# Performance work log

Hardware: AMD Instinct MI355X
Metric: run time of the kernel (lower is better)

Reference implementation:

```python
import jax, jax.numpy as jnp
import numpy as np

D, H, FFN_D, B, LT, LS = 1024, 16, 4096, 4, 1024, 1024
EPS = 1e-5  # torch LayerNorm default
NEG = -10000000000.0


def setup_inputs() -> dict:
    key = jax.random.key(0)
    ks = iter(jax.random.split(key, 64))
    s = 0.02
    n = lambda shape: jax.random.normal(next(ks), shape, jnp.float32) * s
    inp = {
        'enc_output': n((LS, B, D)),
        'embedded': n((LT, B, D)),
        'src_mask': jnp.zeros((LS, B), jnp.bool_),
        'tgt_mask': jnp.zeros((LT, B), jnp.bool_),
    }
    for p in ('mmha', 'ed'):
        for w in ('q', 'k', 'v', 'o'):
            inp[f'{p}_w{w}'] = n((D, D))
            inp[f'{p}_b{w}'] = jnp.zeros((D,), jnp.float32)
    inp['ffn_w1'] = n((FFN_D, D)); inp['ffn_b1'] = jnp.zeros((FFN_D,), jnp.float32)
    inp['ffn_w2'] = n((D, FFN_D)); inp['ffn_b2'] = jnp.zeros((D,), jnp.float32)
    for i in range(3):
        inp[f'ln{i}_g'] = jnp.ones((D,), jnp.float32)
        inp[f'ln{i}_b'] = jnp.zeros((D,), jnp.float32)
    return inp


def _ln(x, g, b):
    m = x.mean(-1, keepdims=True)
    v = ((x - m) ** 2).mean(-1, keepdims=True)
    return (x - m) / jnp.sqrt(v + EPS) * g + b


def _mha(qx, kx, vx, wq, bq, wk, bk, wv, bv, wo, bo, mask):
    # qx: (Lq,B,D); kx,vx: (Lk,B,D); mask broadcastable to (B,H,Lq,Lk), True=masked
    Lq, Bn, Dm = qx.shape
    dk = Dm // H
    proj = lambda x, w, bb: (x @ w.T + bb).reshape(x.shape[0], Bn, H, dk).transpose(1, 2, 0, 3)
    q, k, v = proj(qx, wq, bq), proj(kx, wk, bk), proj(vx, wv, bv)  # (B,H,L,dk)
    scores = jnp.einsum('bhqd,bhkd->bhqk', q, k) / np.float32(np.sqrt(dk))
    scores = jnp.where(mask, NEG, scores)  # masked_fill semantics
    w = jax.nn.softmax(scores, axis=-1)  # dropout is identity in eval
    attn = jnp.einsum('bhqk,bhkd->bhqd', w, v).transpose(2, 0, 1, 3).reshape(Lq, Bn, Dm)
    return attn @ wo.T + bo


def reference(enc_output, embedded, src_mask, tgt_mask,
              mmha_wq, mmha_bq, mmha_wk, mmha_bk, mmha_wv, mmha_bv, mmha_wo, mmha_bo,
              ed_wq, ed_bq, ed_wk, ed_bk, ed_wv, ed_bv, ed_wo, ed_bo,
              ffn_w1, ffn_b1, ffn_w2, ffn_b2,
              ln0_g, ln0_b, ln1_g, ln1_b, ln2_g, ln2_b):
    Lt = embedded.shape[0]
    causal = jnp.triu(jnp.ones((Lt, Lt), jnp.bool_), 1)[None, None]      # (1,1,Lt,Lt)
    tmask = tgt_mask.T[:, None, None, :]                                  # (B,1,1,Lt)
    # Sublayer 0: masked self-attention (computed but UNUSED downstream,
    # faithfully mirroring the original forward which discards self_attn).
    self_attn = embedded + _mha(_ln(embedded, ln0_g, ln0_b), _ln(embedded, ln0_g, ln0_b), _ln(embedded, ln0_g, ln0_b),
                                mmha_wq, mmha_bq, mmha_wk, mmha_bk, mmha_wv, mmha_bv, mmha_wo, mmha_bo,
                                causal | tmask)
    del self_attn
    # Sublayer 1: enc-dec attention; residual input is `embedded` (as in source).
    smask = src_mask.T[:, None, None, :]                                  # (B,1,1,Ls)
    q_in = _ln(embedded, ln1_g, ln1_b)
    enc_dec = embedded + _mha(q_in, enc_output, enc_output,
                              ed_wq, ed_bq, ed_wk, ed_bk, ed_wv, ed_bv, ed_wo, ed_bo,
                              smask)
    # Sublayer 2: FFN
    z = _ln(enc_dec, ln2_g, ln2_b)
    ffn = jnp.maximum(z @ ffn_w1.T + ffn_b1, 0.0) @ ffn_w2.T + ffn_b2
    return enc_dec + ffn
```

## Files before the change

kernel.cpp:

```cpp
#include <hip/hip_runtime.h>
#include <cstdint>
#include <math.h>

constexpr int NH  = 16;
constexpr int DKH = 64;
constexpr int SEQ = 1024;
constexpr int NB  = 4;
constexpr int DM  = 1024;
constexpr int DF  = 4096;

typedef __bf16 bf16;
typedef __bf16 bf16x4 __attribute__((ext_vector_type(4)));
typedef __bf16 bf16x8 __attribute__((ext_vector_type(8)));
typedef float  f32x4  __attribute__((ext_vector_type(4)));

#define MFMA16(a, b, c) __builtin_amdgcn_mfma_f32_16x16x32_bf16((a), (b), (c), 0, 0, 0)

__device__ __forceinline__ void gload_lds16(const void* g, void* l) {
  __builtin_amdgcn_global_load_lds(
      (const __attribute__((address_space(1))) unsigned int*)(uintptr_t)g,
      (__attribute__((address_space(3))) unsigned int*)(uintptr_t)l,
      16, 0, 0);
}

template <int N>
__device__ __forceinline__ void wait_vmcnt() {
  if constexpr (N == 0)      asm volatile("s_waitcnt vmcnt(0)" ::: "memory");
  else if constexpr (N == 3) asm volatile("s_waitcnt vmcnt(3)" ::: "memory");
  else if constexpr (N == 4) asm volatile("s_waitcnt vmcnt(4)" ::: "memory");
  else if constexpr (N == 6) asm volatile("s_waitcnt vmcnt(6)" ::: "memory");
  else                       asm volatile("s_waitcnt vmcnt(8)" ::: "memory");
}

__device__ __forceinline__ int swz32(int row) { return (row >> 1) & 3; }

template <int ROWS>
__device__ __forceinline__ void stage_tile32(const bf16* __restrict__ g, int ldg,
                                             bf16* __restrict__ l, int t) {
  constexpr int ITER = ROWS * 32 / 2048;
#pragma unroll
  for (int i = 0; i < ITER; ++i) {
    const int off = (i * 256 + t) * 8;
    const int row = off >> 5;
    const int cc = (off & 31) >> 3;
    const int sc = cc ^ swz32(row);
    gload_lds16(&g[(size_t)row * ldg + (sc << 3)], &l[off]);
  }
}

__device__ __forceinline__ int rpk(int row, int col) {
  return row * 256 + ((((col >> 3) ^ (row & 7)) << 4)) + ((col & 7) << 1);
}

__global__ __launch_bounds__(256) void prep_kernel(
    const float* __restrict__ wq, const float* __restrict__ wk,
    const float* __restrict__ wv, const float* __restrict__ wo,
    const float* __restrict__ w1, const float* __restrict__ w2,
    const float* __restrict__ enc, const float* __restrict__ emb,
    const float* __restrict__ g1, const float* __restrict__ be1,
    bf16* __restrict__ wqkv_bf, bf16* __restrict__ wo_bf,
    bf16* __restrict__ w1_bf, bf16* __restrict__ w2_bf,
    bf16* __restrict__ enc_bf, bf16* __restrict__ qin_bf) {
  const int bid = blockIdx.x, t = threadIdx.x;
  if (bid < 16384) {
    const float* in;
    bf16* out;
    int idx;
    if (bid < 4096) {
      const int sel = bid >> 10;
      in = sel == 0 ? wq : sel == 1 ? wk : sel == 2 ? wv : wo;
      out = sel == 3 ? wo_bf : wqkv_bf + ((size_t)sel << 20);
      idx = (bid & 1023) * 256 + t;
    } else {
      const int sel = (bid - 4096) >> 12;
      in = sel == 0 ? w1 : sel == 1 ? w2 : enc;
      out = sel == 0 ? w1_bf : sel == 1 ? w2_bf : enc_bf;
      idx = ((bid - 4096) & 4095) * 256 + t;
    }
    const float4 v = ((const float4*)in)[idx];
    bf16x4 ov;
    ov[0] = (bf16)v.x; ov[1] = (bf16)v.y; ov[2] = (bf16)v.z; ov[3] = (bf16)v.w;
    ((bf16x4*)out)[idx] = ov;
    return;
  }
  const int row = bid - 16384;
  const float4 v = ((const float4*)(emb + (size_t)row * DM))[t];
  float s  = v.x + v.y + v.z + v.w;
  float s2 = v.x * v.x + v.y * v.y + v.z * v.z + v.w * v.w;
#pragma unroll
  for (int m = 1; m < 64; m <<= 1) { s += __shfl_xor(s, m); s2 += __shfl_xor(s2, m); }
  __shared__ float red[8];
  const int w = t >> 6;
  if ((t & 63) == 0) { red[w] = s; red[4 + w] = s2; }
  __syncthreads();
  s  = red[0] + red[1] + red[2] + red[3];
  s2 = red[4] + red[5] + red[6] + red[7];
  const float mean = s * (1.f / DM);
  const float var  = s2 * (1.f / DM) - mean * mean;
  const float rstd = rsqrtf(var + 1e-5f);
  const float4 g4 = ((const float4*)g1)[t];
  const float4 b4 = ((const float4*)be1)[t];
  bf16x4 ov;
  ov[0] = (bf16)((v.x - mean) * rstd * g4.x + b4.x);
  ov[1] = (bf16)((v.y - mean) * rstd * g4.y + b4.y);
  ov[2] = (bf16)((v.z - mean) * rstd * g4.z + b4.z);
  ov[3] = (bf16)((v.w - mean) * rstd * g4.w + b4.w);
  ((bf16x4*)(qin_bf + (size_t)row * DM))[t] = ov;
}

__global__ __launch_bounds__(256) void ln_kernel(const float* __restrict__ x,
                                                 const float* __restrict__ gam,
                                                 const float* __restrict__ bet,
                                                 bf16* __restrict__ out) {
  const int row = blockIdx.x, t = threadIdx.x;
  const float4 v = ((const float4*)(x + (size_t)row * DM))[t];
  float s  = v.x + v.y + v.z + v.w;
  float s2 = v.x * v.x + v.y * v.y + v.z * v.z + v.w * v.w;
#pragma unroll
  for (int m = 1; m < 64; m <<= 1) { s += __shfl_xor(s, m); s2 += __shfl_xor(s2, m); }
  __shared__ float red[8];
  const int w = t >> 6;
  if ((t & 63) == 0) { red[w] = s; red[4 + w] = s2; }
  __syncthreads();
  s  = red[0] + red[1] + red[2] + red[3];
  s2 = red[4] + red[5] + red[6] + red[7];
  const float mean = s * (1.f / DM);
  const float var  = s2 * (1.f / DM) - mean * mean;
  const float rstd = rsqrtf(var + 1e-5f);
  const float4 g4 = ((const float4*)gam)[t];
  const float4 b4 = ((const float4*)bet)[t];
  bf16x4 ov;
  ov[0] = (bf16)((v.x - mean) * rstd * g4.x + b4.x);
  ov[1] = (bf16)((v.y - mean) * rstd * g4.y + b4.y);
  ov[2] = (bf16)((v.z - mean) * rstd * g4.z + b4.z);
  ov[3] = (bf16)((v.w - mean) * rstd * g4.w + b4.w);
  ((bf16x4*)(out + (size_t)row * DM))[t] = ov;
}

enum { EPI_QKV = 0, EPI_O = 3, EPI_F1 = 4, EPI_F2 = 5 };

struct GParams {
  const bf16* A;
  const bf16* A2;
  const bf16* W;
  const float* b0;
  const float* b1;
  const float* b2;
  const float* resid;
  void* out;
  void* out1;
  void* out2;
  int N;
  int K;
};

template <int MODE, int BN, int MINB>
__global__ __launch_bounds__(256, MINB) void gemm3(GParams p) {
  constexpr int BM = 128, BK = 32;
  constexpr int WTM = (BN == 128) ? 64 : 32;
  constexpr int MI = WTM / 16;
  constexpr int L = 2 + BN * BK / 2048;
  __shared__ __align__(16) bf16 As[4][BM * BK];
  __shared__ __align__(16) bf16 Bs[4][BN * BK];
  const int t = threadIdx.x, lane = t & 63, w = t >> 6;
  const int lr = lane & 15, lg = lane >> 4;
  const int wr = (BN == 128) ? (w >> 1) : w;
  const int wc = (BN == 128) ? (w & 1) : 0;
  const int m0 = blockIdx.x * BM, n0 = blockIdx.y * BN;
  const bf16* Ap = (MODE == EPI_QKV && n0 >= 1024) ? p.A2 : p.A;
  const bf16* Wp = &p.W[(size_t)n0 * p.K];
  const bf16* Arow = &Ap[(size_t)m0 * p.K];
  const f32x4 FZ = {0.f, 0.f, 0.f, 0.f};
  f32x4 acc[MI][4];
#pragma unroll
  for (int i = 0; i < MI; ++i)
#pragma unroll
    for (int j = 0; j < 4; ++j) acc[i][j] = FZ;

  const int nk = p.K / BK;
  stage_tile32<BM>(Arow, p.K, As[0], t);
  stage_tile32<BN>(Wp, p.K, Bs[0], t);
  stage_tile32<BM>(Arow + BK, p.K, As[1], t);
  stage_tile32<BN>(Wp + BK, p.K, Bs[1], t);

  for (int kt = 0; kt < nk; ++kt) {
    if (kt + 2 < nk) {
      stage_tile32<BM>(Arow + (size_t)(kt + 2) * BK, p.K, As[(kt + 2) & 3], t);
      stage_tile32<BN>(Wp + (size_t)(kt + 2) * BK, p.K, Bs[(kt + 2) & 3], t);
      wait_vmcnt<2 * L>();
    } else if (kt + 1 < nk) {
      wait_vmcnt<L>();
    } else {
      wait_vmcnt<0>();
    }
    __builtin_amdgcn_s_barrier();

    const bf16* Asl = As[kt & 3];
    const bf16* Bsl = Bs[kt & 3];
    bf16x8 af[MI], bfr[4];
#pragma unroll
    for (int i = 0; i < MI; ++i) {
      const int row = wr * WTM + i * 16 + lr;
      af[i] = *(const bf16x8*)&Asl[row * BK + ((lg ^ swz32(row)) << 3)];
    }
#pragma unroll
    for (int j = 0; j < 4; ++j) {
      const int row = wc * 64 + j * 16 + lr;
      bfr[j] = *(const bf16x8*)&Bsl[row * BK + ((lg ^ swz32(row)) << 3)];
    }
    __builtin_amdgcn_s_setprio(1);
#pragma unroll
    for (int i = 0; i < MI; ++i)
#pragma unroll
      for (int j = 0; j < 4; ++j) acc[i][j] = MFMA16(af[i], bfr[j], acc[i][j]);
    __builtin_amdgcn_s_setprio(0);
  }

  if constexpr (BN == 64) {
#pragma unroll
    for (int i = 0; i < MI; ++i) {
#pragma unroll
      for (int j = 0; j < 4; ++j) {
        const int c = n0 + j * 16 + lr;
        const float bj = p.b0[c];
#pragma unroll
        for (int g = 0; g < 4; ++g) {
          const int r = m0 + wr * WTM + i * 16 + 4 * lg + g;
          const size_t idx = (size_t)r * p.N + c;
          ((float*)p.out)[idx] = acc[i][j][g] + bj + p.resid[idx];
        }
      }
    }
    return;
  }

  bf16* R = &As[0][0];
  __syncthreads();
#pragma unroll
  for (int i = 0; i < MI; ++i) {
#pragma unroll
    for (int j = 0; j < 4; ++j) {
      const int col = wc * 64 + j * 16 + lr;
      const int c = n0 + col;
      float bj;
      if constexpr (MODE == EPI_QKV)
        bj = (c < 1024 ? p.b0 : c < 2048 ? p.b1 : p.b2)[c & 1023];
      else
        bj = p.b0[c];
#pragma unroll
      for (int g = 0; g < 4; ++g) {
        const int row = wr * 64 + i * 16 + 4 * lg + g;
        float v = acc[i][j][g] + bj;
        if constexpr (MODE == EPI_QKV) {
          if (c < 1024) v *= 0.125f;
        } else {
          v = fmaxf(v, 0.f);
        }
        *(bf16*)((char*)R + rpk(row, col)) = (bf16)v;
      }
    }
  }
  __syncthreads();

  if constexpr (MODE == EPI_F1) {
#pragma unroll
    for (int q = 0; q < 8; ++q) {
      const int idx = q * 256 + t;
      const int r = idx >> 4, cc = idx & 15;
      const bf16x8 vv = *(const bf16x8*)((char*)R + r * 256 + (((cc ^ (r & 7)) << 4)));
      *(bf16x8*)&((bf16*)p.out)[(size_t)(m0 + r) * p.N + n0 + cc * 8] = vv;
    }
  } else {
    const int l0 = m0 >> 2;
    const int h0 = (n0 & 1023) >> 6;
    if (n0 < 2048) {
      bf16* outp = (bf16*)(n0 < 1024 ? p.out : p.out1);
#pragma unroll
      for (int q = 0; q < 8; ++q) {
        const int b = q >> 1, hsel = q & 1;
        const int l = t >> 3, cc = t & 7;
        const int row = l * 4 + b;
        const int ccl = hsel * 8 + cc;
        const bf16x8 vv = *(const bf16x8*)((char*)R + row * 256 + (((ccl ^ (row & 7)) << 4)));
        const int bh = b * NH + h0 + hsel;
        *(bf16x8*)&outp[(((size_t)bh << 10) + l0 + l) * DKH + cc * 8] = vv;
      }
    } else {
      bf16* outp = (bf16*)p.out2;
#pragma unroll
      for (int q = 0; q < 8; ++q) {
        const int idx = q * 256 + t;
        const int rs = idx >> 2, kc = idx & 3;
        const int b = rs >> 7, hsel = (rs >> 6) & 1, d = rs & 63;
        const int col = hsel * 64 + d;
        bf16x8 vv;
#pragma unroll
        for (int e = 0; e < 8; ++e) {
          const int row = (kc * 8 + e) * 4 + b;
          vv[e] = *(const bf16*)((char*)R + rpk(row, col));
        }
        const int bh = b * NH + h0 + hsel;
        *(bf16x8*)&outp[(((size_t)bh * DKH + d) << 10) + l0 + kc * 8] = vv;
      }
    }
  }
}

__global__ __launch_bounds__(512, 4) void attn_kernel(const bf16* __restrict__ Qg,
                                                      const bf16* __restrict__ Kg,
                                                      const bf16* __restrict__ Vtg,
                                                      const unsigned char* __restrict__ smask,
                                                      bf16* __restrict__ Og) {
  __shared__ __align__(16) bf16 Ks[2][4096];
  __shared__ __align__(16) bf16 Vs[2][4096];
  __shared__ __align__(16) bf16 Ps[8][1152];
  const int t = threadIdx.x, lane = t & 63, w = t >> 6;
  const int lr = lane & 15, lg = lane >> 4;
  const int id = blockIdx.x;
  const int bh = ((id >> 6) << 3) | (id & 7);
  const int qt = (id >> 3) & 7;
  const int b = bh >> 4, h = bh & 15;
  const int q0 = qt * 128 + w * 16;
  const size_t base = (size_t)bh << 16;

  bf16x8 qa[2];
#pragma unroll
  for (int c = 0; c < 2; ++c)
    qa[c] = *(const bf16x8*)&Qg[base + (size_t)(q0 + lr) * DKH + c * 32 + lg * 8];

  const f32x4 FZ = {0.f, 0.f, 0.f, 0.f};
  f32x4 o[4];
  float mrun[4], lrun[4];
#pragma unroll
  for (int g = 0; g < 4; ++g) { mrun[g] = -INFINITY; lrun[g] = 0.f; o[g] = FZ; }

  const int soff = t * 8;
  const int shi = soff >> 11, smid = (soff >> 5) & 63;
  const int ssc = (((soff >> 3) & 3) ^ ((smid >> 1) & 3)) << 3;

  gload_lds16(&Kg[base + (size_t)smid * DKH + shi * 32 + ssc], &Ks[0][soff]);
  gload_lds16(&Vtg[base + (size_t)smid * SEQ + shi * 32 + ssc], &Vs[0][soff]);
  asm volatile("s_waitcnt vmcnt(0)" ::: "memory");
  __syncthreads();

  const int rsw = ((lr >> 1) & 3);

  int cur = 0;
  for (int kt = 0; kt < SEQ / 64; ++kt) {
    const int kv0 = kt * 64;
    if (kt + 1 < SEQ / 64) {
      gload_lds16(&Kg[base + (size_t)(kv0 + 64 + smid) * DKH + shi * 32 + ssc], &Ks[cur ^ 1][soff]);
      gload_lds16(&Vtg[base + (size_t)smid * SEQ + kv0 + 64 + shi * 32 + ssc], &Vs[cur ^ 1][soff]);
    }

    f32x4 s[4];
#pragma unroll
    for (int n = 0; n < 4; ++n) s[n] = FZ;
#pragma unroll
    for (int c = 0; c < 2; ++c) {
      bf16x8 kb[4];
#pragma unroll
      for (int n = 0; n < 4; ++n)
        kb[n] = *(const bf16x8*)&Ks[cur][c * 2048 + (n * 16 + lr) * 32 + ((lg ^ rsw) << 3)];
      __builtin_amdgcn_s_setprio(1);
#pragma unroll
      for (int n = 0; n < 4; ++n) s[n] = MFMA16(qa[c], kb[n], s[n]);
      __builtin_amdgcn_s_setprio(0);
    }

    float madd[4];
#pragma unroll
    for (int n = 0; n < 4; ++n)
      madd[n] = smask[(size_t)(kv0 + n * 16 + lr) * NB + b] ? -1e10f : 0.f;
#pragma unroll
    for (int n = 0; n < 4; ++n)
#pragma unroll
      for (int g = 0; g < 4; ++g) s[n][g] += madd[n];

    float tm4[4];
    bool needany = false;
#pragma unroll
    for (int g = 0; g < 4; ++g) {
      float tm = fmaxf(fmaxf(s[0][g], s[1][g]), fmaxf(s[2][g], s[3][g]));
      tm = fmaxf(tm, __shfl_xor(tm, 1));
      tm = fmaxf(tm, __shfl_xor(tm, 2));
      tm = fmaxf(tm, __shfl_xor(tm, 4));
      tm = fmaxf(tm, __shfl_xor(tm, 8));
      tm4[g] = tm;
      needany |= (tm > mrun[g] + 8.f);
    }
    if (__any(needany)) {
#pragma unroll
      for (int g = 0; g < 4; ++g) {
        const float mnew = fmaxf(mrun[g], tm4[g]);
        const float sc = __expf(mrun[g] - mnew);
        mrun[g] = mnew;
        lrun[g] *= sc;
#pragma unroll
        for (int n = 0; n < 4; ++n) o[n][g] *= sc;
      }
    }
#pragma unroll
    for (int g = 0; g < 4; ++g) {
      float ts = 0.f;
#pragma unroll
      for (int n = 0; n < 4; ++n) {
        const float p = __expf(s[n][g] - mrun[g]);
        s[n][g] = p;
        ts += p;
      }
      ts += __shfl_xor(ts, 1);
      ts += __shfl_xor(ts, 2);
      ts += __shfl_xor(ts, 4);
      ts += __shfl_xor(ts, 8);
      lrun[g] += ts;
    }

    bf16* Pw = &Ps[w][0];
#pragma unroll
    for (int n = 0; n < 4; ++n)
#pragma unroll
      for (int g = 0; g < 4; ++g)
        Pw[(4 * lg + g) * 72 + n * 16 + lr] = (bf16)s[n][g];
    __builtin_amdgcn_sched_barrier(0);

#pragma unroll
    for (int c = 0; c < 2; ++c) {
      const bf16x8 pa = *(const bf16x8*)&Pw[lr * 72 + c * 32 + lg * 8];
      bf16x8 vb[4];
#pragma unroll
      for (int n = 0; n < 4; ++n)
        vb[n] = *(const bf16x8*)&Vs[cur][c * 2048 + (n * 16 + lr) * 32 + ((lg ^ rsw) << 3)];
      __builtin_amdgcn_s_setprio(1);
#pragma unroll
      for (int n = 0; n < 4; ++n) o[n] = MFMA16(pa, vb[n], o[n]);
      __builtin_amdgcn_s_setprio(0);
    }

    asm volatile("s_waitcnt vmcnt(0)" ::: "memory");
    __syncthreads();
    cur ^= 1;
  }

#pragma unroll
  for (int g = 0; g < 4; ++g) {
    const int l = q0 + 4 * lg + g;
    const float inv = 1.0f / lrun[g];
#pragma unroll
    for (int n = 0; n < 4; ++n)
      Og[(size_t)(l * NB + b) * DM + h * 64 + n * 16 + lr] = (bf16)(o[n][g] * inv);
  }
}

extern "C" void kernel_launch(void* const* d_in, const int* in_sizes, int n_in,
                              void* d_out, int out_size, void* d_ws, size_t ws_size,
                              hipStream_t stream) {
  const float* enc = (const float*)d_in[0];
  const float* emb = (const float*)d_in[1];
  const unsigned char* smask = (const unsigned char*)d_in[2];
  const float* wq = (const float*)d_in[12]; const float* bq = (const float*)d_in[13];
  const float* wk = (const float*)d_in[14]; const float* bk = (const float*)d_in[15];
  const float* wv = (const float*)d_in[16]; const float* bv = (const float*)d_in[17];
  const float* wo = (const float*)d_in[18]; const float* bo = (const float*)d_in[19];
  const float* w1 = (const float*)d_in[20]; const float* b1 = (const float*)d_in[21];
  const float* w2 = (const float*)d_in[22]; const float* b2 = (const float*)d_in[23];
  const float* g1 = (const float*)d_in[26]; const float* be1 = (const float*)d_in[27];
  const float* g2 = (const float*)d_in[28]; const float* be2 = (const float*)d_in[29];

  char* ws = (char*)d_ws;
  const size_t MB = (size_t)1 << 20;
  bf16* wqkv_bf = (bf16*)(ws + 0 * MB);
  bf16* wo_bf   = (bf16*)(ws + 6 * MB);
  bf16* w1_bf   = (bf16*)(ws + 8 * MB);
  bf16* w2_bf   = (bf16*)(ws + 16 * MB);
  bf16* enc_bf  = (bf16*)(ws + 24 * MB);
  bf16* z_bf    = enc_bf;
  bf16* qin_bf  = (bf16*)(ws + 32 * MB);
  bf16* attn_bf = qin_bf;
  bf16* Q_bf    = (bf16*)(ws + 40 * MB);
  bf16* K_bf    = (bf16*)(ws + 48 * MB);
  bf16* Vt_bf   = (bf16*)(ws + 56 * MB);
  float* encdec = (float*)(ws + 64 * MB);
  bf16* h_bf    = (bf16*)(ws + 80 * MB);

  prep_kernel<<<20480, 256, 0, stream>>>(wq, wk, wv, wo, w1, w2, enc, emb, g1, be1,
                                         wqkv_bf, wo_bf, w1_bf, w2_bf, enc_bf, qin_bf);

  {
    GParams p{qin_bf, enc_bf, wqkv_bf, bq, bk, bv, nullptr, Q_bf, K_bf, Vt_bf, 3072, DM};
    gemm3<EPI_QKV, 128, 2><<<dim3(32, 24), 256, 0, stream>>>(p);
  }

  attn_kernel<<<512, 512, 0, stream>>>(Q_bf, K_bf, Vt_bf, smask, attn_bf);

  {
    GParams p{attn_bf, nullptr, wo_bf, bo, nullptr, nullptr, emb, encdec, nullptr, nullptr, DM, DM};
    gemm3<EPI_O, 64, 3><<<dim3(32, 16), 256, 0, stream>>>(p);
  }

  ln_kernel<<<4096, 256, 0, stream>>>(encdec, g2, be2, z_bf);

  {
    GParams p{z_bf, nullptr, w1_bf, b1, nullptr, nullptr, nullptr, h_bf, nullptr, nullptr, DF, DM};
    gemm3<EPI_F1, 128, 2><<<dim3(32, 32), 256, 0, stream>>>(p);
  }
  {
    GParams p{h_bf, nullptr, w2_bf, b2, nullptr, nullptr, encdec, d_out, nullptr, nullptr, DM, DF};
    gemm3<EPI_F2, 64, 3><<<dim3(32, 16), 256, 0, stream>>>(p);
  }
}
```

Before: 395.8 us.

## Use 256x128x64 GEMM tiles with split-K partials for O-proj and FFN2

Replaces the 128-row, BK=32, 4-stage GEMM with a 512-thread kernel using 256x128 tiles, BK=64 and a 3-buffer pipeline with 8-way XOR swizzle. The O-projection and second FFN GEMM become split-K=2 kernels that write fp32 partials. The partials are summed with bias and residual in the LayerNorm kernel and in a new finalize kernel. This raises data reuse per tile and keeps the N=1024 GEMMs filling the GPU, at the cost of extra fp32 partial traffic and an added elementwise kernel.

```diff
diff --git a/kernel.cpp b/kernel.cpp
--- a/kernel.cpp
+++ b/kernel.cpp
@@ -26,30 +26,25 @@
 template <int N>
 __device__ __forceinline__ void wait_vmcnt() {
   if constexpr (N == 0)      asm volatile("s_waitcnt vmcnt(0)" ::: "memory");
-  else if constexpr (N == 3) asm volatile("s_waitcnt vmcnt(3)" ::: "memory");
-  else if constexpr (N == 4) asm volatile("s_waitcnt vmcnt(4)" ::: "memory");
   else if constexpr (N == 6) asm volatile("s_waitcnt vmcnt(6)" ::: "memory");
-  else                       asm volatile("s_waitcnt vmcnt(8)" ::: "memory");
-}
-
-__device__ __forceinline__ int swz32(int row) { return (row >> 1) & 3; }
-
-template <int ROWS>
-__device__ __forceinline__ void stage_tile32(const bf16* __restrict__ g, int ldg,
-                                             bf16* __restrict__ l, int t) {
-  constexpr int ITER = ROWS * 32 / 2048;
-#pragma unroll
-  for (int i = 0; i < ITER; ++i) {
-    const int off = (i * 256 + t) * 8;
-    const int row = off >> 5;
-    const int cc = (off & 31) >> 3;
-    const int sc = cc ^ swz32(row);
-    gload_lds16(&g[(size_t)row * ldg + (sc << 3)], &l[off]);
+  else                       asm volatile("s_waitcnt vmcnt(12)" ::: "memory");
+}
+
+template <int R>
+__device__ __forceinline__ void stage64(const bf16* __restrict__ g, int ldg,
+                                        bf16* __restrict__ l, int t) {
+#pragma unroll
+  for (int i = 0; i < R / 64; ++i) {
+    const int off = (i * 512 + t) * 16;
+    const int row = off >> 7;
+    const int cc = (off >> 4) & 7;
+    const int sc = cc ^ (row & 7);
+    gload_lds16(&g[(size_t)row * ldg + sc * 8], (char*)l + off);
   }
 }
 
 __device__ __forceinline__ int rpk(int row, int col) {
-  return row * 256 + ((((col >> 3) ^ (row & 7)) << 4)) + ((col & 7) << 1);
+  return row * 256 + (((col >> 3) ^ (row & 7)) << 4) + ((col & 7) << 1);
 }
 
 __global__ __launch_bounds__(256) void prep_kernel(
@@ -108,12 +103,25 @@
   ((bf16x4*)(qin_bf + (size_t)row * DM))[t] = ov;
 }
 
-__global__ __launch_bounds__(256) void ln_kernel(const float* __restrict__ x,
-                                                 const float* __restrict__ gam,
-                                                 const float* __restrict__ bet,
-                                                 bf16* __restrict__ out) {
+__global__ __launch_bounds__(256) void ln2_kernel(const float* __restrict__ P0,
+                                                  const float* __restrict__ P1,
+                                                  const float* __restrict__ bo,
+                                                  const float* __restrict__ emb,
+                                                  const float* __restrict__ gam,
+                                                  const float* __restrict__ bet,
+                                                  float* __restrict__ encdec,
+                                                  bf16* __restrict__ z) {
   const int row = blockIdx.x, t = threadIdx.x;
-  const float4 v = ((const float4*)(x + (size_t)row * DM))[t];
+  const float4 p0 = ((const float4*)(P0 + (size_t)row * DM))[t];
+  const float4 p1 = ((const float4*)(P1 + (size_t)row * DM))[t];
+  const float4 e4 = ((const float4*)(emb + (size_t)row * DM))[t];
+  const float4 bb = ((const float4*)bo)[t];
+  float4 v;
+  v.x = p0.x + p1.x + bb.x + e4.x;
+  v.y = p0.y + p1.y + bb.y + e4.y;
+  v.z = p0.z + p1.z + bb.z + e4.z;
+  v.w = p0.w + p1.w + bb.w + e4.w;
+  ((float4*)(encdec + (size_t)row * DM))[t] = v;
   float s  = v.x + v.y + v.z + v.w;
   float s2 = v.x * v.x + v.y * v.y + v.z * v.z + v.w * v.w;
 #pragma unroll
@@ -134,173 +142,183 @@
   ov[1] = (bf16)((v.y - mean) * rstd * g4.y + b4.y);
   ov[2] = (bf16)((v.z - mean) * rstd * g4.z + b4.z);
   ov[3] = (bf16)((v.w - mean) * rstd * g4.w + b4.w);
-  ((bf16x4*)(out + (size_t)row * DM))[t] = ov;
-}
-
-enum { EPI_QKV = 0, EPI_O = 3, EPI_F1 = 4, EPI_F2 = 5 };
-
-struct GParams {
+  ((bf16x4*)(z + (size_t)row * DM))[t] = ov;
+}
+
+__global__ __launch_bounds__(256) void fin_kernel(const float* __restrict__ P0,
+                                                  const float* __restrict__ P1,
+                                                  const float* __restrict__ b2,
+                                                  const float* __restrict__ encdec,
+                                                  float* __restrict__ out) {
+  const int idx = blockIdx.x * 256 + threadIdx.x;
+  const float4 p0 = ((const float4*)P0)[idx];
+  const float4 p1 = ((const float4*)P1)[idx];
+  const float4 e4 = ((const float4*)encdec)[idx];
+  const float4 bb = ((const float4*)b2)[idx & 255];
+  float4 v;
+  v.x = p0.x + p1.x + bb.x + e4.x;
+  v.y = p0.y + p1.y + bb.y + e4.y;
+  v.z = p0.z + p1.z + bb.z + e4.z;
+  v.w = p0.w + p1.w + bb.w + e4.w;
+  ((float4*)out)[idx] = v;
+}
+
+enum { G_QKV = 0, G_F1 = 1, G_PART = 2 };
+
+struct GP {
   const bf16* A;
   const bf16* A2;
   const bf16* W;
   const float* b0;
   const float* b1;
   const float* b2;
-  const float* resid;
   void* out;
   void* out1;
   void* out2;
   int N;
   int K;
+  int Ksl;
 };
 
-template <int MODE, int BN, int MINB>
-__global__ __launch_bounds__(256, MINB) void gemm3(GParams p) {
-  constexpr int BM = 128, BK = 32;
-  constexpr int WTM = (BN == 128) ? 64 : 32;
-  constexpr int MI = WTM / 16;
-  constexpr int L = 2 + BN * BK / 2048;
-  __shared__ __align__(16) bf16 As[4][BM * BK];
-  __shared__ __align__(16) bf16 Bs[4][BN * BK];
+template <int MODE>
+__global__ __launch_bounds__(512, 1) void gemm4(GP p) {
+  constexpr int BM = 256, BN = 128, BK = 64;
+  __shared__ __align__(16) bf16 As[3][BM * BK];
+  __shared__ __align__(16) bf16 Bs[3][BN * BK];
   const int t = threadIdx.x, lane = t & 63, w = t >> 6;
   const int lr = lane & 15, lg = lane >> 4;
-  const int wr = (BN == 128) ? (w >> 1) : w;
-  const int wc = (BN == 128) ? (w & 1) : 0;
+  const int wr = w >> 1, wc = w & 1;
   const int m0 = blockIdx.x * BM, n0 = blockIdx.y * BN;
-  const bf16* Ap = (MODE == EPI_QKV && n0 >= 1024) ? p.A2 : p.A;
-  const bf16* Wp = &p.W[(size_t)n0 * p.K];
-  const bf16* Arow = &Ap[(size_t)m0 * p.K];
+  const bf16* Ap = (MODE == G_QKV && n0 >= 1024) ? p.A2 : p.A;
+  const bf16* Arow = Ap + (size_t)m0 * p.K + (size_t)blockIdx.z * p.Ksl;
+  const bf16* Wrow = p.W + (size_t)n0 * p.K + (size_t)blockIdx.z * p.Ksl;
   const f32x4 FZ = {0.f, 0.f, 0.f, 0.f};
-  f32x4 acc[MI][4];
-#pragma unroll
-  for (int i = 0; i < MI; ++i)
+  f32x4 acc[4][4];
+#pragma unroll
+  for (int i = 0; i < 4; ++i)
 #pragma unroll
     for (int j = 0; j < 4; ++j) acc[i][j] = FZ;
 
-  const int nk = p.K / BK;
-  stage_tile32<BM>(Arow, p.K, As[0], t);
-  stage_tile32<BN>(Wp, p.K, Bs[0], t);
-  stage_tile32<BM>(Arow + BK, p.K, As[1], t);
-  stage_tile32<BN>(Wp + BK, p.K, Bs[1], t);
-
+  const int nk = p.Ksl / BK;
+  stage64<BM>(Arow, p.K, As[0], t);
+  stage64<BN>(Wrow, p.K, Bs[0], t);
+
+  int bi = 0;
   for (int kt = 0; kt < nk; ++kt) {
-    if (kt + 2 < nk) {
-      stage_tile32<BM>(Arow + (size_t)(kt + 2) * BK, p.K, As[(kt + 2) & 3], t);
-      stage_tile32<BN>(Wp + (size_t)(kt + 2) * BK, p.K, Bs[(kt + 2) & 3], t);
-      wait_vmcnt<2 * L>();
-    } else if (kt + 1 < nk) {
-      wait_vmcnt<L>();
+    int si = bi + 1; if (si == 3) si = 0;
+    if (kt + 1 < nk) {
+      stage64<BM>(Arow + (size_t)(kt + 1) * BK, p.K, As[si], t);
+      stage64<BN>(Wrow + (size_t)(kt + 1) * BK, p.K, Bs[si], t);
+      wait_vmcnt<6>();
     } else {
       wait_vmcnt<0>();
     }
     __builtin_amdgcn_s_barrier();
 
-    const bf16* Asl = As[kt & 3];
-    const bf16* Bsl = Bs[kt & 3];
-    bf16x8 af[MI], bfr[4];
-#pragma unroll
-    for (int i = 0; i < MI; ++i) {
-      const int row = wr * WTM + i * 16 + lr;
-      af[i] = *(const bf16x8*)&Asl[row * BK + ((lg ^ swz32(row)) << 3)];
-    }
+    const bf16* Asl = As[bi];
+    const bf16* Bsl = Bs[bi];
+#pragma unroll
+    for (int kh = 0; kh < 2; ++kh) {
+      bf16x8 af[4], bfr[4];
+#pragma unroll
+      for (int i = 0; i < 4; ++i) {
+        const int row = wr * 64 + i * 16 + lr;
+        af[i] = *(const bf16x8*)((const char*)Asl + row * 128 + ((((kh * 4 + lg) ^ (row & 7))) << 4));
+      }
+#pragma unroll
+      for (int j = 0; j < 4; ++j) {
+        const int row = wc * 64 + j * 16 + lr;
+        bfr[j] = *(const bf16x8*)((const char*)Bsl + row * 128 + ((((kh * 4 + lg) ^ (row & 7))) << 4));
+      }
+      __builtin_amdgcn_s_setprio(1);
+#pragma unroll
+      for (int i = 0; i < 4; ++i)
+#pragma unroll
+        for (int j = 0; j < 4; ++j) acc[i][j] = MFMA16(af[i], bfr[j], acc[i][j]);
+      __builtin_amdgcn_s_setprio(0);
+    }
+    bi = si;
+  }
+
+  if constexpr (MODE == G_PART) {
+    float* Op = (float*)p.out + (size_t)blockIdx.z * ((size_t)4096 * p.N);
+#pragma unroll
+    for (int i = 0; i < 4; ++i)
+#pragma unroll
+      for (int j = 0; j < 4; ++j) {
+        const int c = n0 + wc * 64 + j * 16 + lr;
+#pragma unroll
+        for (int g = 0; g < 4; ++g) {
+          const int r = m0 + wr * 64 + i * 16 + 4 * lg + g;
+          Op[(size_t)r * p.N + c] = acc[i][j][g];
+        }
+      }
+    return;
+  }
+
+  bf16* R = As[0];
+  __syncthreads();
+#pragma unroll
+  for (int i = 0; i < 4; ++i)
 #pragma unroll
     for (int j = 0; j < 4; ++j) {
-      const int row = wc * 64 + j * 16 + lr;
-      bfr[j] = *(const bf16x8*)&Bsl[row * BK + ((lg ^ swz32(row)) << 3)];
-    }
-    __builtin_amdgcn_s_setprio(1);
-#pragma unroll
-    for (int i = 0; i < MI; ++i)
-#pragma unroll
-      for (int j = 0; j < 4; ++j) acc[i][j] = MFMA16(af[i], bfr[j], acc[i][j]);
-    __builtin_amdgcn_s_setprio(0);
-  }
-
-  if constexpr (BN == 64) {
-#pragma unroll
-    for (int i = 0; i < MI; ++i) {
-#pragma unroll
-      for (int j = 0; j < 4; ++j) {
-        const int c = n0 + j * 16 + lr;
-        const float bj = p.b0[c];
-#pragma unroll
-        for (int g = 0; g < 4; ++g) {
-          const int r = m0 + wr * WTM + i * 16 + 4 * lg + g;
-          const size_t idx = (size_t)r * p.N + c;
-          ((float*)p.out)[idx] = acc[i][j][g] + bj + p.resid[idx];
-        }
-      }
-    }
-    return;
-  }
-
-  bf16* R = &As[0][0];
-  __syncthreads();
-#pragma unroll
-  for (int i = 0; i < MI; ++i) {
-#pragma unroll
-    for (int j = 0; j < 4; ++j) {
-      const int col = wc * 64 + j * 16 + lr;
-      const int c = n0 + col;
+      const int cl = wc * 64 + j * 16 + lr;
+      const int c = n0 + cl;
       float bj;
-      if constexpr (MODE == EPI_QKV)
+      if constexpr (MODE == G_QKV)
         bj = (c < 1024 ? p.b0 : c < 2048 ? p.b1 : p.b2)[c & 1023];
       else
         bj = p.b0[c];
 #pragma unroll
       for (int g = 0; g < 4; ++g) {
-        const int row = wr * 64 + i * 16 + 4 * lg + g;
+        const int rl = wr * 64 + i * 16 + 4 * lg + g;
         float v = acc[i][j][g] + bj;
-        if constexpr (MODE == EPI_QKV) {
+        if constexpr (MODE == G_QKV) {
           if (c < 1024) v *= 0.125f;
         } else {
           v = fmaxf(v, 0.f);
         }
-        *(bf16*)((char*)R + rpk(row, col)) = (bf16)v;
-      }
-    }
-  }
+        *(bf16*)((char*)R + rpk(rl, cl)) = (bf16)v;
+      }
+    }
   __syncthreads();
 
-  if constexpr (MODE == EPI_F1) {
+  if constexpr (MODE == G_F1) {
 #pragma unroll
     for (int q = 0; q < 8; ++q) {
-      const int idx = q * 256 + t;
-      const int r = idx >> 4, cc = idx & 15;
-      const bf16x8 vv = *(const bf16x8*)((char*)R + r * 256 + (((cc ^ (r & 7)) << 4)));
-      *(bf16x8*)&((bf16*)p.out)[(size_t)(m0 + r) * p.N + n0 + cc * 8] = vv;
+      const int idx = q * 512 + t;
+      const int ch = idx & 15, row = idx >> 4;
+      const bf16x8 vv = *(const bf16x8*)((char*)R + row * 256 + ((ch ^ (row & 7)) << 4));
+      *(bf16x8*)&((bf16*)p.out)[(size_t)(m0 + row) * p.N + n0 + ch * 8] = vv;
     }
   } else {
     const int l0 = m0 >> 2;
-    const int h0 = (n0 & 1023) >> 6;
     if (n0 < 2048) {
       bf16* outp = (bf16*)(n0 < 1024 ? p.out : p.out1);
+      const int h0 = (n0 & 1023) >> 6;
 #pragma unroll
       for (int q = 0; q < 8; ++q) {
-        const int b = q >> 1, hsel = q & 1;
-        const int l = t >> 3, cc = t & 7;
-        const int row = l * 4 + b;
-        const int ccl = hsel * 8 + cc;
-        const bf16x8 vv = *(const bf16x8*)((char*)R + row * 256 + (((ccl ^ (row & 7)) << 4)));
-        const int bh = b * NH + h0 + hsel;
-        *(bf16x8*)&outp[(((size_t)bh << 10) + l0 + l) * DKH + cc * 8] = vv;
+        const int idx = q * 512 + t;
+        const int dc = idx & 7, ll = (idx >> 3) & 63, b = (idx >> 9) & 3, hs = idx >> 11;
+        const int row = ll * 4 + b, col = hs * 64 + dc * 8;
+        const bf16x8 vv = *(const bf16x8*)((char*)R + row * 256 + ((((col >> 3) ^ (row & 7))) << 4));
+        *(bf16x8*)&outp[((size_t)(b * NH + h0 + hs) * 1024 + l0 + ll) * 64 + dc * 8] = vv;
       }
     } else {
       bf16* outp = (bf16*)p.out2;
+      const int h0 = (n0 - 2048) >> 6;
 #pragma unroll
       for (int q = 0; q < 8; ++q) {
-        const int idx = q * 256 + t;
-        const int rs = idx >> 2, kc = idx & 3;
-        const int b = rs >> 7, hsel = (rs >> 6) & 1, d = rs & 63;
-        const int col = hsel * 64 + d;
+        const int idx = q * 512 + t;
+        const int kc = idx & 7, d = (idx >> 3) & 63, b = (idx >> 9) & 3, hs = idx >> 11;
+        const int col = hs * 64 + d;
         bf16x8 vv;
 #pragma unroll
         for (int e = 0; e < 8; ++e) {
           const int row = (kc * 8 + e) * 4 + b;
           vv[e] = *(const bf16*)((char*)R + rpk(row, col));
         }
-        const int bh = b * NH + h0 + hsel;
-        *(bf16x8*)&outp[(((size_t)bh * DKH + d) << 10) + l0 + kc * 8] = vv;
+        *(bf16x8*)&outp[((size_t)(b * NH + h0 + hs) * 64 + d) * 1024 + l0 + kc * 8] = vv;
       }
     }
   }
@@ -482,30 +500,37 @@
   bf16* Vt_bf   = (bf16*)(ws + 56 * MB);
   float* encdec = (float*)(ws + 64 * MB);
   bf16* h_bf    = (bf16*)(ws + 80 * MB);
+  float* Po     = (float*)(ws + 112 * MB);
+  float* Pf     = (float*)(ws + 112 * MB);
 
   prep_kernel<<<20480, 256, 0, stream>>>(wq, wk, wv, wo, w1, w2, enc, emb, g1, be1,
                                          wqkv_bf, wo_bf, w1_bf, w2_bf, enc_bf, qin_bf);
 
   {
-    GParams p{qin_bf, enc_bf, wqkv_bf, bq, bk, bv, nullptr, Q_bf, K_bf, Vt_bf, 3072, DM};
-    gemm3<EPI_QKV, 128, 2><<<dim3(32, 24), 256, 0, stream>>>(p);
+    GP p{qin_bf, enc_bf, wqkv_bf, bq, bk, bv, Q_bf, K_bf, Vt_bf, 3072, DM, DM};
+    gemm4<G_QKV><<<dim3(16, 24, 1), 512, 0, stream>>>(p);
   }
 
   attn_kernel<<<512, 512, 0, stream>>>(Q_bf, K_bf, Vt_bf, smask, attn_bf);
 
   {
-    GParams p{attn_bf, nullptr, wo_bf, bo, nullptr, nullptr, emb, encdec, nullptr, nullptr, DM, DM};
-    gemm3<EPI_O, 64, 3><<<dim3(32, 16), 256, 0, stream>>>(p);
-  }
-
-  ln_kernel<<<4096, 256, 0, stream>>>(encdec, g2, be2, z_bf);
+    GP p{attn_bf, nullptr, wo_bf, nullptr, nullptr, nullptr, Po, nullptr, nullptr, DM, DM, DM / 2};
+    gemm4<G_PART><<<dim3(16, 8, 2), 512, 0, stream>>>(p);
+  }
+
+  ln2_kernel<<<4096, 256, 0, stream>>>(Po, Po + (size_t)4096 * 1024, bo, emb, g2, be2,
+                                       encdec, z_bf);
 
   {
-    GParams p{z_bf, nullptr, w1_bf, b1, nullptr, nullptr, nullptr, h_bf, nullptr, nullptr, DF, DM};
-    gemm3<EPI_F1, 128, 2><<<dim3(32, 32), 256, 0, stream>>>(p);
-  }
+    GP p{z_bf, nullptr, w1_bf, b1, nullptr, nullptr, h_bf, nullptr, nullptr, DF, DM, DM};
+    gemm4<G_F1><<<dim3(16, 32, 1), 512, 0, stream>>>(p);
+  }
+
   {
-    GParams p{h_bf, nullptr, w2_bf, b2, nullptr, nullptr, encdec, d_out, nullptr, nullptr, DM, DF};
-    gemm3<EPI_F2, 64, 3><<<dim3(32, 16), 256, 0, stream>>>(p);
-  }
-}
+    GP p{h_bf, nullptr, w2_bf, nullptr, nullptr, nullptr, Pf, nullptr, nullptr, DM, DF, DF / 2};
+    gemm4<G_PART><<<dim3(16, 8, 2), 512, 0, stream>>>(p);
+  }
+
+  fin_kernel<<<4096, 256, 0, stream>>>(Pf, Pf + (size_t)4096 * 1024, b2, encdec,
+                                       (float*)d_out);
+}
```

New measurement: 371.0 us. -6.3%, faster.
